# Kernel tuning notes

Measured on AMD Instinct MI355X. Metric: run time of the kernel, lower is better.

Reference implementation:

```python
import jax, jax.numpy as jnp
import numpy as np

B, S, D = 2, 1024, 768      # batch, seq, d_model
F, F_UP = 8192, 8192        # downstream / upstream dictionary sizes
K = 64                      # top-k of the downstream AE
MASK_DENSITY = 0.05         # fraction of allowed feature-feature connections


def setup_inputs() -> dict:
    key = jax.random.key(0)
    ks = jax.random.split(key, 12)
    inv_sqrt_d = 1.0 / np.sqrt(D)
    resid = jax.random.normal(ks[0], (B, S, D), dtype=jnp.float32)
    # upstream pruned features: k-sparse-ish non-negative activations
    pruned0 = jax.nn.relu(jax.random.normal(ks[1], (B, S, F_UP)) - 2.0).astype(jnp.float32)
    pruned1 = jax.nn.relu(jax.random.normal(ks[2], (B, S, F_UP)) - 2.0).astype(jnp.float32)
    feature_buffer = jnp.zeros((B, S, F), dtype=jnp.float32)
    W_enc = jax.random.normal(ks[3], (F, D), dtype=jnp.float32) * inv_sqrt_d
    b_enc = jax.random.normal(ks[4], (F,), dtype=jnp.float32) * 0.01
    W_dec = jax.random.normal(ks[5], (F, D), dtype=jnp.float32) * inv_sqrt_d
    b_dec = jax.random.normal(ks[6], (D,), dtype=jnp.float32) * 0.01
    W_dec_up0 = jax.random.normal(ks[7], (F_UP, D), dtype=jnp.float32) * inv_sqrt_d
    W_dec_up1 = jax.random.normal(ks[8], (F_UP, D), dtype=jnp.float32) * inv_sqrt_d
    b_dec_up0 = jax.random.normal(ks[9], (D,), dtype=jnp.float32) * 0.01
    b_dec_up1 = jax.random.normal(ks[10], (D,), dtype=jnp.float32) * 0.01
    km0, km1 = jax.random.split(ks[11])
    mask0 = (jax.random.uniform(km0, (F, F_UP)) < MASK_DENSITY).astype(jnp.float32)
    mask1 = (jax.random.uniform(km1, (F, F_UP)) < MASK_DENSITY).astype(jnp.float32)
    return {
        "resid": resid, "pruned0": pruned0, "pruned1": pruned1,
        "feature_buffer": feature_buffer,
        "W_enc": W_enc, "b_enc": b_enc, "W_dec": W_dec, "b_dec": b_dec,
        "W_dec_up0": W_dec_up0, "W_dec_up1": W_dec_up1,
        "b_dec_up0": b_dec_up0, "b_dec_up1": b_dec_up1,
        "mask0": mask0, "mask1": mask1, "k": K,
    }


def reference(resid, pruned0, pruned1, feature_buffer,
              W_enc, b_enc, W_dec, b_dec,
              W_dec_up0, W_dec_up1, b_dec_up0, b_dec_up1,
              mask0, mask1, k):
    # initial contributions: encode the cached residual stream, [B,S,F]
    approx = jnp.einsum("bsd,fd->bsf", resid, W_enc)
    upstream_bias = b_dec_up0 + b_dec_up1
    # accumulate connection-masked upstream contributions
    for pruned, W_dec_up, mask in ((pruned0, W_dec_up0, mask0),
                                   (pruned1, W_dec_up1, mask1)):
        # masked virtual weights: [F, F_up]
        virtual = jnp.einsum("fd,ud->fu", W_enc, W_dec_up) * mask
        approx = approx + jnp.einsum("bsu,fu->bsf", pruned, virtual)
    # bias correction: project summed upstream decoder biases, add encoder bias
    approx = approx + jnp.einsum("fd,d->f", W_enc, upstream_bias) + b_enc
    # topk (unsorted set equals torch's sorted=False), relu, scatter into buffer
    top_vals, top_idx = jax.lax.top_k(approx, k)        # [B,S,k]
    top_vals = jax.nn.relu(top_vals)
    Bn, Sn, Fn = feature_buffer.shape
    bi = jnp.arange(Bn)[:, None, None]
    si = jnp.arange(Sn)[None, :, None]
    feat_buffer = jnp.zeros_like(feature_buffer).at[bi, si, top_idx].set(top_vals)
    # dense decode
    reconstructions = jnp.einsum("bsf,fd->bsd", feat_buffer, W_dec) + b_dec
    return feat_buffer, reconstructions
```

## Files before the change

### kernel.cpp

```cpp
#include <hip/hip_runtime.h>
#include <stdint.h>

typedef unsigned long long u64;
typedef unsigned short u16;

#define F_DIM 8192
#define U_DIM 8192
#define D_DIM 768
#define NTOK  2048
#define KSEL  64
#define COLCAP 544
#define TILE  256
#define NFT   32
#define NUT   32
#define DCH   32
#define ENTCAP 3840
#define NBIN  1024

__global__ void k_bias(const float* __restrict__ Wenc, const float* __restrict__ benc,
                       const float* __restrict__ b0, const float* __restrict__ b1,
                       float* __restrict__ t_bias) {
    int wid = threadIdx.x >> 6, lane = threadIdx.x & 63;
    int f = blockIdx.x * 4 + wid;
    const float* row = Wenc + (size_t)f * D_DIM;
    float s = 0.f;
    for (int j = lane; j < D_DIM; j += 64) s += row[j] * (b0[j] + b1[j]);
    #pragma unroll
    for (int off = 32; off; off >>= 1) s += __shfl_down(s, off, 64);
    if (lane == 0) t_bias[f] = s + benc[f];
}

__global__ void k_mask_scan(const float* __restrict__ mask0, const float* __restrict__ mask1,
                            int* __restrict__ cnt_tile, u64* __restrict__ bitmap) {
    int ut = blockIdx.x, ft = blockIdx.y, l = blockIdx.z;
    const float* mask = l ? mask1 : mask0;
    int tid = threadIdx.x, lane = tid & 63, wid = tid >> 6;
    int u = ut * TILE + tid;
    int f0 = ft * TILE;
    u64* bm = bitmap + (((size_t)(l * NFT + ft) * NUT + ut) * TILE) * 4;
    int cnt = 0;
    for (int fl = 0; fl < TILE; ++fl) {
        float v = mask[(size_t)(f0 + fl) * U_DIM + u];
        int nz = (v != 0.0f);
        cnt += nz;
        u64 bal = __ballot(nz);
        if (lane == 0) bm[(size_t)fl * 4 + wid] = bal;
    }
    cnt_tile[(size_t)(l * NFT + ft) * U_DIM + u] = cnt;
}

__global__ void k_col_prefix(const int* __restrict__ cnt_tile, int* __restrict__ base,
                             int* __restrict__ cnt_tot) {
    int idx = blockIdx.x * blockDim.x + threadIdx.x;
    int l = idx >> 13, u = idx & (U_DIM - 1);
    int run = 0;
    for (int ft = 0; ft < NFT; ++ft) {
        int c = cnt_tile[(size_t)(l * NFT + ft) * U_DIM + u];
        base[(size_t)(l * NFT + ft) * U_DIM + u] = run;
        run += c;
    }
    cnt_tot[l * U_DIM + u] = run < COLCAP ? run : COLCAP;
}

__global__ __launch_bounds__(256, 2) void k_virt_build(
        const float* __restrict__ Wenc, const float* __restrict__ Wup0,
        const float* __restrict__ Wup1, const u64* __restrict__ bitmap,
        const int* __restrict__ base, u16* __restrict__ csc_f, float* __restrict__ csc_v) {
    __shared__ u64 bm[TILE][4];
    __shared__ int cs[TILE];
    __shared__ unsigned char entf[ENTCAP];
    __shared__ float acc[ENTCAP];
    __shared__ float we_t[DCH][TILE + 1];
    int ut = blockIdx.x, ft = blockIdx.y, l = blockIdx.z;
    const float* Wup = l ? Wup1 : Wup0;
    int tid = threadIdx.x;
    int u0 = ut * TILE, f0 = ft * TILE;

    const u64* gbm = bitmap + (((size_t)(l * NFT + ft) * NUT + ut) * TILE) * 4;
    for (int i = tid; i < TILE * 4; i += 256) ((u64*)bm)[i] = gbm[i];
    __syncthreads();

    int w = tid >> 6, b = tid & 63;
    int cnt = 0;
    for (int fl = 0; fl < TILE; ++fl) cnt += (int)((bm[fl][w] >> b) & 1ULL);
    cs[tid] = cnt;
    __syncthreads();
    for (int off = 1; off < 256; off <<= 1) {
        int v = (tid >= off) ? cs[tid - off] : 0;
        __syncthreads();
        cs[tid] += v;
        __syncthreads();
    }
    int cstart = cs[tid] - cnt;
    {
        int i = 0;
        for (int fl = 0; fl < TILE; ++fl)
            if ((bm[fl][w] >> b) & 1ULL) {
                int p = cstart + i;
                if (p < ENTCAP) entf[p] = (unsigned char)fl;
                ++i;
            }
    }
    for (int i = tid; i < ENTCAP; i += 256) acc[i] = 0.f;
    __syncthreads();

    float wu[DCH];
    for (int d0 = 0; d0 < D_DIM; d0 += DCH) {
        const float* wr = Wenc + (size_t)(f0 + tid) * D_DIM + d0;
        #pragma unroll
        for (int j = 0; j < DCH; j += 4) {
            float4 t4 = *(const float4*)(wr + j);
            we_t[j][tid] = t4.x; we_t[j + 1][tid] = t4.y;
            we_t[j + 2][tid] = t4.z; we_t[j + 3][tid] = t4.w;
        }
        const float* ur = Wup + (size_t)(u0 + tid) * D_DIM + d0;
        #pragma unroll
        for (int j = 0; j < DCH; j += 4) {
            float4 t4 = *(const float4*)(ur + j);
            wu[j] = t4.x; wu[j + 1] = t4.y; wu[j + 2] = t4.z; wu[j + 3] = t4.w;
        }
        __syncthreads();
        for (int i = 0; i < cnt; ++i) {
            int p = cstart + i;
            if (p >= ENTCAP) break;
            int fl = entf[p];
            float s = 0.f;
            #pragma unroll
            for (int j = 0; j < DCH; ++j) s += we_t[j][fl] * wu[j];
            acc[p] += s;
        }
        __syncthreads();
    }
    int u = u0 + tid;
    int bse = base[(size_t)(l * NFT + ft) * U_DIM + u];
    size_t colbase = ((size_t)l * U_DIM + u) * COLCAP;
    for (int i = 0; i < cnt; ++i) {
        int p = cstart + i;
        if (p >= ENTCAP) break;
        int slot = bse + i;
        if (slot < COLCAP) {
            csc_f[colbase + slot] = (u16)(f0 + entf[p]);
            csc_v[colbase + slot] = acc[p];
        }
    }
}

__global__ __launch_bounds__(512) void k_contrib(
        const float* __restrict__ pruned0, const float* __restrict__ pruned1,
        const int* __restrict__ cnt_tot, const u16* __restrict__ csc_f,
        const float* __restrict__ csc_v, float* __restrict__ C) {
    __shared__ float accum[F_DIM];
    int t = blockIdx.x;
    int tid = threadIdx.x, lane = tid & 63, wid = tid >> 6;
    for (int i = tid; i < F_DIM; i += 512) accum[i] = 0.f;
    __syncthreads();
    for (int l = 0; l < 2; ++l) {
        const float* P = (l ? pruned1 : pruned0) + (size_t)t * U_DIM;
        const int* cl = cnt_tot + l * U_DIM;
        const u16* cf = csc_f + (size_t)l * U_DIM * COLCAP;
        const float* cv = csc_v + (size_t)l * U_DIM * COLCAP;
        for (int w = wid; w < U_DIM / 64; w += 8) {
            float pv = P[w * 64 + lane];
            u64 bal = __ballot(pv != 0.0f);
            while (bal) {
                int bb = __builtin_ctzll(bal);
                bal &= bal - 1;
                int u = w * 64 + bb;
                float p = __shfl(pv, bb, 64);
                int cn = cl[u];
                size_t cb = (size_t)u * COLCAP;
                for (int e = lane; e < cn; e += 64) {
                    int f = cf[cb + e];
                    float v = cv[cb + e];
                    atomicAdd(&accum[f], p * v);
                }
            }
        }
    }
    __syncthreads();
    float* Crow = C + (size_t)t * F_DIM;
    for (int i = tid; i < F_DIM; i += 512) Crow[i] = accum[i];
}

#define BM 128
#define BN 128
#define BK 16
__global__ __launch_bounds__(256) void k_encoder(
        const float* __restrict__ resid, const float* __restrict__ Wenc,
        const float* __restrict__ t_bias, float* __restrict__ C) {
    __shared__ float As[BK][BM + 4];
    __shared__ float Bs[BK][BN + 4];
    int tid = threadIdx.x;
    int m0 = blockIdx.y * BM, n0 = blockIdx.x * BN;
    int mt = tid & 15, nt = tid >> 4;
    float acc[8][8] = {};
    for (int k0 = 0; k0 < D_DIM; k0 += BK) {
        if (tid < 128) {
            const float* ar = resid + (size_t)(m0 + tid) * D_DIM + k0;
            #pragma unroll
            for (int j = 0; j < BK; j += 4) {
                float4 t4 = *(const float4*)(ar + j);
                As[j][tid] = t4.x; As[j + 1][tid] = t4.y;
                As[j + 2][tid] = t4.z; As[j + 3][tid] = t4.w;
            }
        } else {
            int r = tid - 128;
            const float* br = Wenc + (size_t)(n0 + r) * D_DIM + k0;
            #pragma unroll
            for (int j = 0; j < BK; j += 4) {
                float4 t4 = *(const float4*)(br + j);
                Bs[j][r] = t4.x; Bs[j + 1][r] = t4.y;
                Bs[j + 2][r] = t4.z; Bs[j + 3][r] = t4.w;
            }
        }
        __syncthreads();
        #pragma unroll
        for (int k = 0; k < BK; ++k) {
            float a[8], bb[8];
            *(float4*)&a[0]  = *(const float4*)&As[k][mt * 8];
            *(float4*)&a[4]  = *(const float4*)&As[k][mt * 8 + 4];
            *(float4*)&bb[0] = *(const float4*)&Bs[k][nt * 8];
            *(float4*)&bb[4] = *(const float4*)&Bs[k][nt * 8 + 4];
            #pragma unroll
            for (int i = 0; i < 8; ++i)
                #pragma unroll
                for (int j = 0; j < 8; ++j) acc[i][j] += a[i] * bb[j];
        }
        __syncthreads();
    }
    float tb[8];
    #pragma unroll
    for (int j = 0; j < 8; ++j) tb[j] = t_bias[n0 + nt * 8 + j];
    #pragma unroll
    for (int i = 0; i < 8; ++i) {
        float* cr = C + (size_t)(m0 + mt * 8 + i) * F_DIM + n0 + nt * 8;
        #pragma unroll
        for (int j = 0; j < 8; ++j) cr[j] += acc[i][j] + tb[j];
    }
}

__global__ __launch_bounds__(256) void k_select(
        float* __restrict__ C, int* __restrict__ sel_idx, float* __restrict__ sel_val) {
    __shared__ float row[F_DIM];
    __shared__ int hist[NBIN];
    __shared__ int bstar, nsure, ncand;
    __shared__ float sure_v[64];  __shared__ int sure_f[64];
    __shared__ float cand_v[256]; __shared__ int cand_f[256];
    __shared__ float out_v[KSEL]; __shared__ int out_f[KSEL];
    int t = blockIdx.x, tid = threadIdx.x;
    float* Crow = C + (size_t)t * F_DIM;
    for (int i = tid; i < F_DIM; i += 256) row[i] = Crow[i];
    for (int i = tid; i < NBIN; i += 256) hist[i] = 0;
    __syncthreads();
    for (int i = tid; i < F_DIM; i += 256) {
        int b = (int)floorf((row[i] + 16.0f) * 32.0f);
        b = b < 0 ? 0 : (b > NBIN - 1 ? NBIN - 1 : b);
        atomicAdd(&hist[b], 1);
    }
    __syncthreads();
    if (tid == 0) {
        int cum = 0, bs = 0;
        for (int b = NBIN - 1; b >= 0; --b) { cum += hist[b]; if (cum >= KSEL) { bs = b; break; } }
        bstar = bs; nsure = 0; ncand = 0;
    }
    __syncthreads();
    int bs = bstar;
    for (int i = tid; i < F_DIM; i += 256) {
        float v = row[i];
        int b = (int)floorf((v + 16.0f) * 32.0f);
        b = b < 0 ? 0 : (b > NBIN - 1 ? NBIN - 1 : b);
        if (b > bs) {
            int p = atomicAdd(&nsure, 1);
            if (p < 64) { sure_v[p] = v; sure_f[p] = i; }
        } else if (b == bs) {
            int p = atomicAdd(&ncand, 1);
            if (p < 256) { cand_v[p] = v; cand_f[p] = i; }
        }
    }
    __syncthreads();
    if (tid == 0) {
        int c1 = nsure; if (c1 > KSEL) c1 = KSEL;
        for (int i = 0; i < c1; ++i) { out_v[i] = sure_v[i]; out_f[i] = sure_f[i]; }
        int need = KSEL - c1;
        int nc = ncand; if (nc > 256) nc = 256;
        for (int s = 0; s < need; ++s) {
            float bv = -1e30f; int bf = 0x7fffffff, bi = -1;
            for (int i = 0; i < nc; ++i) {
                float v = cand_v[i];
                if (v > bv || (v == bv && cand_f[i] < bf)) { bv = v; bf = cand_f[i]; bi = i; }
            }
            if (bi < 0) { out_v[c1 + s] = 0.f; out_f[c1 + s] = 0; continue; }
            out_v[c1 + s] = cand_v[bi]; out_f[c1 + s] = cand_f[bi];
            cand_v[bi] = -1e30f;
        }
    }
    __syncthreads();
    for (int i = tid; i < F_DIM; i += 256) Crow[i] = 0.0f;
    __syncthreads();
    if (tid < KSEL) {
        float v = out_v[tid]; int f = out_f[tid];
        float rv = v > 0.f ? v : 0.f;
        Crow[f] = rv;
        sel_idx[t * KSEL + tid] = f;
        sel_val[t * KSEL + tid] = rv;
    }
}

__global__ __launch_bounds__(256) void k_decode(
        const int* __restrict__ sel_idx, const float* __restrict__ sel_val,
        const float* __restrict__ Wdec, const float* __restrict__ bdec,
        float* __restrict__ recon) {
    __shared__ int sf[KSEL]; __shared__ float sv[KSEL];
    int t = blockIdx.x, tid = threadIdx.x;
    if (tid < KSEL) { sf[tid] = sel_idx[t * KSEL + tid]; sv[tid] = sel_val[t * KSEL + tid]; }
    __syncthreads();
    for (int d = tid; d < D_DIM; d += 256) {
        float s = bdec[d];
        #pragma unroll 8
        for (int j = 0; j < KSEL; ++j) s += sv[j] * Wdec[(size_t)sf[j] * D_DIM + d];
        recon[(size_t)t * D_DIM + d] = s;
    }
}

extern "C" void kernel_launch(void* const* d_in, const int* in_sizes, int n_in,
                              void* d_out, int out_size, void* d_ws, size_t ws_size,
                              hipStream_t stream) {
    (void)in_sizes; (void)n_in; (void)out_size; (void)ws_size;
    const float* resid   = (const float*)d_in[0];
    const float* pruned0 = (const float*)d_in[1];
    const float* pruned1 = (const float*)d_in[2];
    const float* Wenc    = (const float*)d_in[4];
    const float* benc    = (const float*)d_in[5];
    const float* Wdec    = (const float*)d_in[6];
    const float* bdec    = (const float*)d_in[7];
    const float* Wup0    = (const float*)d_in[8];
    const float* Wup1    = (const float*)d_in[9];
    const float* bup0    = (const float*)d_in[10];
    const float* bup1    = (const float*)d_in[11];
    const float* mask0   = (const float*)d_in[12];
    const float* mask1   = (const float*)d_in[13];

    char* ws = (char*)d_ws;
    size_t o = 0;
    auto alloc = [&](size_t bytes) -> char* {
        o = (o + 255) & ~(size_t)255;
        char* p = ws + o; o += bytes; return p;
    };
    float* t_bias   = (float*)alloc((size_t)F_DIM * 4);
    int*   cnt_tile = (int*)  alloc((size_t)2 * NFT * U_DIM * 4);
    int*   basep    = (int*)  alloc((size_t)2 * NFT * U_DIM * 4);
    int*   cnt_tot  = (int*)  alloc((size_t)2 * U_DIM * 4);
    u64*   bitmap   = (u64*)  alloc((size_t)2 * NFT * NUT * TILE * 4 * 8);
    u16*   csc_f    = (u16*)  alloc((size_t)2 * U_DIM * COLCAP * 2);
    float* csc_v    = (float*)alloc((size_t)2 * U_DIM * COLCAP * 4);
    int*   sel_idx  = (int*)  alloc((size_t)NTOK * KSEL * 4);
    float* sel_val  = (float*)alloc((size_t)NTOK * KSEL * 4);

    float* out   = (float*)d_out;
    float* C     = out;
    float* recon = out + (size_t)NTOK * F_DIM;

    hipLaunchKernelGGL(k_bias,       dim3(F_DIM / 4),        dim3(256), 0, stream,
                       Wenc, benc, bup0, bup1, t_bias);
    hipLaunchKernelGGL(k_mask_scan,  dim3(NUT, NFT, 2),      dim3(256), 0, stream,
                       mask0, mask1, cnt_tile, bitmap);
    hipLaunchKernelGGL(k_col_prefix, dim3(2 * U_DIM / 256),  dim3(256), 0, stream,
                       cnt_tile, basep, cnt_tot);
    hipLaunchKernelGGL(k_virt_build, dim3(NUT, NFT, 2),      dim3(256), 0, stream,
                       Wenc, Wup0, Wup1, bitmap, basep, csc_f, csc_v);
    hipLaunchKernelGGL(k_contrib,    dim3(NTOK),             dim3(512), 0, stream,
                       pruned0, pruned1, cnt_tot, csc_f, csc_v, C);
    hipLaunchKernelGGL(k_encoder,    dim3(F_DIM / BN, NTOK / BM), dim3(256), 0, stream,
                       resid, Wenc, t_bias, C);
    hipLaunchKernelGGL(k_select,     dim3(NTOK),             dim3(256), 0, stream,
                       C, sel_idx, sel_val);
    hipLaunchKernelGGL(k_decode,     dim3(NTOK),             dim3(256), 0, stream,
                       sel_idx, sel_val, Wdec, bdec, recon);
}
```

Measured before the change: 4.322 ms.

## Switch virtual weights to CSR and compute upstream contributions per token-tile/feature-tile

Rebuilds the masked virtual weight matrix as row-major CSR (per downstream feature) instead of CSC, and adds a kernel that collects, for each 128-token tile, a capped list of (token, value) pairs of nonzero upstream activations per upstream feature. The contribution kernel now processes a 128x128 token-by-feature tile in shared memory, walking each feature's CSR row and that tile's token lists, with an XCD-aware block mapping. This is meant to replace a per-token scan of whole CSC columns with scattered atomics over 8192 features by tile-local accumulation with better reuse. The per-tile token list is capped at 16 entries per upstream feature, which may silently drop contributions if activations are denser than expected, and shared-memory atomics remain.

```diff
diff --git a/kernel.cpp b/kernel.cpp
--- a/kernel.cpp
+++ b/kernel.cpp
@@ -9,13 +9,17 @@
 #define D_DIM 768
 #define NTOK  2048
 #define KSEL  64
-#define COLCAP 544
+#define ROWCAP 544
 #define TILE  256
 #define NFT   32
 #define NUT   32
 #define DCH   32
 #define ENTCAP 3840
 #define NBIN  1024
+#define FT    128
+#define TT    128
+#define NTT   16
+#define PCAP  16
 
 __global__ void k_bias(const float* __restrict__ Wenc, const float* __restrict__ benc,
                        const float* __restrict__ b0, const float* __restrict__ b1,
@@ -31,46 +35,46 @@
 }
 
 __global__ void k_mask_scan(const float* __restrict__ mask0, const float* __restrict__ mask1,
-                            int* __restrict__ cnt_tile, u64* __restrict__ bitmap) {
+                            int* __restrict__ rowcnt_tile, u64* __restrict__ bitmap) {
+    __shared__ int rc[TILE][4];
     int ut = blockIdx.x, ft = blockIdx.y, l = blockIdx.z;
     const float* mask = l ? mask1 : mask0;
     int tid = threadIdx.x, lane = tid & 63, wid = tid >> 6;
     int u = ut * TILE + tid;
     int f0 = ft * TILE;
     u64* bm = bitmap + (((size_t)(l * NFT + ft) * NUT + ut) * TILE) * 4;
-    int cnt = 0;
     for (int fl = 0; fl < TILE; ++fl) {
         float v = mask[(size_t)(f0 + fl) * U_DIM + u];
-        int nz = (v != 0.0f);
-        cnt += nz;
-        u64 bal = __ballot(nz);
-        if (lane == 0) bm[(size_t)fl * 4 + wid] = bal;
-    }
-    cnt_tile[(size_t)(l * NFT + ft) * U_DIM + u] = cnt;
-}
-
-__global__ void k_col_prefix(const int* __restrict__ cnt_tile, int* __restrict__ base,
-                             int* __restrict__ cnt_tot) {
+        u64 bal = __ballot(v != 0.0f);
+        if (lane == 0) { bm[(size_t)fl * 4 + wid] = bal; rc[fl][wid] = __popcll(bal); }
+    }
+    __syncthreads();
+    rowcnt_tile[(size_t)(l * NUT + ut) * F_DIM + f0 + tid] =
+        rc[tid][0] + rc[tid][1] + rc[tid][2] + rc[tid][3];
+}
+
+__global__ void k_row_prefix(const int* __restrict__ rowcnt_tile, int* __restrict__ base_r,
+                             int* __restrict__ rowcnt_tot) {
     int idx = blockIdx.x * blockDim.x + threadIdx.x;
-    int l = idx >> 13, u = idx & (U_DIM - 1);
+    int l = idx >> 13, f = idx & (F_DIM - 1);
     int run = 0;
-    for (int ft = 0; ft < NFT; ++ft) {
-        int c = cnt_tile[(size_t)(l * NFT + ft) * U_DIM + u];
-        base[(size_t)(l * NFT + ft) * U_DIM + u] = run;
+    for (int ut = 0; ut < NUT; ++ut) {
+        int c = rowcnt_tile[(size_t)(l * NUT + ut) * F_DIM + f];
+        base_r[(size_t)(l * NUT + ut) * F_DIM + f] = run;
         run += c;
     }
-    cnt_tot[l * U_DIM + u] = run < COLCAP ? run : COLCAP;
+    rowcnt_tot[l * F_DIM + f] = run < ROWCAP ? run : ROWCAP;
 }
 
 __global__ __launch_bounds__(256, 2) void k_virt_build(
         const float* __restrict__ Wenc, const float* __restrict__ Wup0,
         const float* __restrict__ Wup1, const u64* __restrict__ bitmap,
-        const int* __restrict__ base, u16* __restrict__ csc_f, float* __restrict__ csc_v) {
+        const int* __restrict__ base_r, u16* __restrict__ csr_u, float* __restrict__ csr_v) {
     __shared__ u64 bm[TILE][4];
     __shared__ int cs[TILE];
-    __shared__ unsigned char entf[ENTCAP];
+    __shared__ unsigned char entu[ENTCAP];
     __shared__ float acc[ENTCAP];
-    __shared__ float we_t[DCH][TILE + 1];
+    __shared__ float wu_t[DCH][TILE + 1];
     int ut = blockIdx.x, ft = blockIdx.y, l = blockIdx.z;
     const float* Wup = l ? Wup1 : Wup0;
     int tid = threadIdx.x;
@@ -80,9 +84,9 @@
     for (int i = tid; i < TILE * 4; i += 256) ((u64*)bm)[i] = gbm[i];
     __syncthreads();
 
-    int w = tid >> 6, b = tid & 63;
     int cnt = 0;
-    for (int fl = 0; fl < TILE; ++fl) cnt += (int)((bm[fl][w] >> b) & 1ULL);
+    #pragma unroll
+    for (int w = 0; w < 4; ++w) cnt += (int)__popcll(bm[tid][w]);
     cs[tid] = cnt;
     __syncthreads();
     for (int off = 1; off < 256; off <<= 1) {
@@ -94,92 +98,131 @@
     int cstart = cs[tid] - cnt;
     {
         int i = 0;
-        for (int fl = 0; fl < TILE; ++fl)
-            if ((bm[fl][w] >> b) & 1ULL) {
+        #pragma unroll
+        for (int w = 0; w < 4; ++w) {
+            u64 word = bm[tid][w];
+            while (word) {
+                int b = __builtin_ctzll(word); word &= word - 1;
                 int p = cstart + i;
-                if (p < ENTCAP) entf[p] = (unsigned char)fl;
+                if (p < ENTCAP) entu[p] = (unsigned char)(w * 64 + b);
                 ++i;
             }
+        }
     }
     for (int i = tid; i < ENTCAP; i += 256) acc[i] = 0.f;
     __syncthreads();
 
-    float wu[DCH];
+    float we[DCH];
     for (int d0 = 0; d0 < D_DIM; d0 += DCH) {
+        const float* ur = Wup + (size_t)(u0 + tid) * D_DIM + d0;
+        #pragma unroll
+        for (int j = 0; j < DCH; j += 4) {
+            float4 t4 = *(const float4*)(ur + j);
+            wu_t[j][tid] = t4.x; wu_t[j + 1][tid] = t4.y;
+            wu_t[j + 2][tid] = t4.z; wu_t[j + 3][tid] = t4.w;
+        }
         const float* wr = Wenc + (size_t)(f0 + tid) * D_DIM + d0;
         #pragma unroll
         for (int j = 0; j < DCH; j += 4) {
             float4 t4 = *(const float4*)(wr + j);
-            we_t[j][tid] = t4.x; we_t[j + 1][tid] = t4.y;
-            we_t[j + 2][tid] = t4.z; we_t[j + 3][tid] = t4.w;
-        }
-        const float* ur = Wup + (size_t)(u0 + tid) * D_DIM + d0;
-        #pragma unroll
-        for (int j = 0; j < DCH; j += 4) {
-            float4 t4 = *(const float4*)(ur + j);
-            wu[j] = t4.x; wu[j + 1] = t4.y; wu[j + 2] = t4.z; wu[j + 3] = t4.w;
+            we[j] = t4.x; we[j + 1] = t4.y; we[j + 2] = t4.z; we[j + 3] = t4.w;
         }
         __syncthreads();
         for (int i = 0; i < cnt; ++i) {
             int p = cstart + i;
             if (p >= ENTCAP) break;
-            int fl = entf[p];
+            int ul = entu[p];
             float s = 0.f;
             #pragma unroll
-            for (int j = 0; j < DCH; ++j) s += we_t[j][fl] * wu[j];
+            for (int j = 0; j < DCH; ++j) s += we[j] * wu_t[j][ul];
             acc[p] += s;
         }
         __syncthreads();
     }
-    int u = u0 + tid;
-    int bse = base[(size_t)(l * NFT + ft) * U_DIM + u];
-    size_t colbase = ((size_t)l * U_DIM + u) * COLCAP;
+    int f = f0 + tid;
+    int bse = base_r[(size_t)(l * NUT + ut) * F_DIM + f];
+    size_t rb = ((size_t)l * F_DIM + f) * ROWCAP;
     for (int i = 0; i < cnt; ++i) {
         int p = cstart + i;
         if (p >= ENTCAP) break;
         int slot = bse + i;
-        if (slot < COLCAP) {
-            csc_f[colbase + slot] = (u16)(f0 + entf[p]);
-            csc_v[colbase + slot] = acc[p];
-        }
-    }
-}
-
-__global__ __launch_bounds__(512) void k_contrib(
+        if (slot < ROWCAP) {
+            csr_u[rb + slot] = (u16)(u0 + entu[p]);
+            csr_v[rb + slot] = acc[p];
+        }
+    }
+}
+
+__global__ __launch_bounds__(256) void k_ptok(
         const float* __restrict__ pruned0, const float* __restrict__ pruned1,
-        const int* __restrict__ cnt_tot, const u16* __restrict__ csc_f,
-        const float* __restrict__ csc_v, float* __restrict__ C) {
-    __shared__ float accum[F_DIM];
-    int t = blockIdx.x;
+        u64* __restrict__ lists, unsigned char* __restrict__ cnt8) {
+    __shared__ int cl[U_DIM];
+    int tt = blockIdx.x, l = blockIdx.y;
+    int tid = threadIdx.x;
+    for (int i = tid; i < U_DIM; i += 256) cl[i] = 0;
+    __syncthreads();
+    const float* P = (l ? pruned1 : pruned0) + (size_t)tt * TT * U_DIM;
+    u64* L = lists + (size_t)(l * NTT + tt) * U_DIM * PCAP;
+    for (int t = 0; t < TT; ++t) {
+        const float* Pr = P + (size_t)t * U_DIM;
+        for (int u = tid; u < U_DIM; u += 256) {
+            float v = Pr[u];
+            if (v != 0.0f) {
+                int c = atomicAdd(&cl[u], 1);
+                if (c < PCAP)
+                    L[(size_t)u * PCAP + c] = ((u64)__float_as_uint(v) << 32) | (unsigned)t;
+            }
+        }
+    }
+    __syncthreads();
+    unsigned char* C8 = cnt8 + (size_t)(l * NTT + tt) * U_DIM;
+    for (int u = tid; u < U_DIM; u += 256) {
+        int c = cl[u];
+        C8[u] = (unsigned char)(c < PCAP ? c : PCAP);
+    }
+}
+
+__global__ __launch_bounds__(512, 2) void k_contrib2(
+        const u16* __restrict__ csr_u, const float* __restrict__ csr_v,
+        const int* __restrict__ rowcnt_tot, const u64* __restrict__ lists,
+        const unsigned char* __restrict__ cnt8, float* __restrict__ C) {
+    __shared__ float accum[TT][FT + 1];
+    __shared__ unsigned char lc[U_DIM];
+    int raw = blockIdx.x;
+    int xcd = raw & 7, idx = raw >> 3;
+    int ft = (xcd << 3) | (idx & 7);
+    int tt = idx >> 3;
     int tid = threadIdx.x, lane = tid & 63, wid = tid >> 6;
-    for (int i = tid; i < F_DIM; i += 512) accum[i] = 0.f;
-    __syncthreads();
+    for (int i = tid; i < TT * (FT + 1); i += 512) ((float*)accum)[i] = 0.f;
     for (int l = 0; l < 2; ++l) {
-        const float* P = (l ? pruned1 : pruned0) + (size_t)t * U_DIM;
-        const int* cl = cnt_tot + l * U_DIM;
-        const u16* cf = csc_f + (size_t)l * U_DIM * COLCAP;
-        const float* cv = csc_v + (size_t)l * U_DIM * COLCAP;
-        for (int w = wid; w < U_DIM / 64; w += 8) {
-            float pv = P[w * 64 + lane];
-            u64 bal = __ballot(pv != 0.0f);
-            while (bal) {
-                int bb = __builtin_ctzll(bal);
-                bal &= bal - 1;
-                int u = w * 64 + bb;
-                float p = __shfl(pv, bb, 64);
-                int cn = cl[u];
-                size_t cb = (size_t)u * COLCAP;
-                for (int e = lane; e < cn; e += 64) {
-                    int f = cf[cb + e];
-                    float v = cv[cb + e];
-                    atomicAdd(&accum[f], p * v);
+        __syncthreads();
+        for (int i = tid; i < U_DIM; i += 512) lc[i] = cnt8[(size_t)(l * NTT + tt) * U_DIM + i];
+        __syncthreads();
+        const u64* L = lists + (size_t)(l * NTT + tt) * U_DIM * PCAP;
+        for (int r = wid; r < FT; r += 8) {
+            int f = ft * FT + r;
+            int cnt = rowcnt_tot[l * F_DIM + f];
+            size_t rb = ((size_t)l * F_DIM + f) * ROWCAP;
+            for (int e = lane; e < cnt; e += 64) {
+                int u = csr_u[rb + e];
+                float v = csr_v[rb + e];
+                int c = lc[u];
+                const u64* lp = L + (size_t)u * PCAP;
+                for (int j = 0; j < c; ++j) {
+                    u64 pk = lp[j];
+                    int tok = (int)(unsigned)pk;
+                    float p = __uint_as_float((unsigned)(pk >> 32));
+                    atomicAdd(&accum[tok][r], p * v);
                 }
             }
         }
     }
     __syncthreads();
-    float* Crow = C + (size_t)t * F_DIM;
-    for (int i = tid; i < F_DIM; i += 512) Crow[i] = accum[i];
+    int t0 = tt * TT, f0 = ft * FT;
+    for (int i = tid; i < TT * FT; i += 512) {
+        int tok = i >> 7, r = i & (FT - 1);
+        C[(size_t)(t0 + tok) * F_DIM + f0 + r] = accum[tok][r];
+    }
 }
 
 #define BM 128
@@ -346,15 +389,17 @@
         o = (o + 255) & ~(size_t)255;
         char* p = ws + o; o += bytes; return p;
     };
-    float* t_bias   = (float*)alloc((size_t)F_DIM * 4);
-    int*   cnt_tile = (int*)  alloc((size_t)2 * NFT * U_DIM * 4);
-    int*   basep    = (int*)  alloc((size_t)2 * NFT * U_DIM * 4);
-    int*   cnt_tot  = (int*)  alloc((size_t)2 * U_DIM * 4);
-    u64*   bitmap   = (u64*)  alloc((size_t)2 * NFT * NUT * TILE * 4 * 8);
-    u16*   csc_f    = (u16*)  alloc((size_t)2 * U_DIM * COLCAP * 2);
-    float* csc_v    = (float*)alloc((size_t)2 * U_DIM * COLCAP * 4);
-    int*   sel_idx  = (int*)  alloc((size_t)NTOK * KSEL * 4);
-    float* sel_val  = (float*)alloc((size_t)NTOK * KSEL * 4);
+    float* t_bias      = (float*)alloc((size_t)F_DIM * 4);
+    int*   rowcnt_tile = (int*)  alloc((size_t)2 * NUT * F_DIM * 4);
+    int*   base_r      = (int*)  alloc((size_t)2 * NUT * F_DIM * 4);
+    int*   rowcnt_tot  = (int*)  alloc((size_t)2 * F_DIM * 4);
+    u64*   bitmap      = (u64*)  alloc((size_t)2 * NFT * NUT * TILE * 4 * 8);
+    u16*   csr_u       = (u16*)  alloc((size_t)2 * F_DIM * ROWCAP * 2);
+    float* csr_v       = (float*)alloc((size_t)2 * F_DIM * ROWCAP * 4);
+    u64*   lists       = (u64*)  alloc((size_t)2 * NTT * U_DIM * PCAP * 8);
+    unsigned char* cnt8 = (unsigned char*)alloc((size_t)2 * NTT * U_DIM);
+    int*   sel_idx     = (int*)  alloc((size_t)NTOK * KSEL * 4);
+    float* sel_val     = (float*)alloc((size_t)NTOK * KSEL * 4);
 
     float* out   = (float*)d_out;
     float* C     = out;
@@ -363,13 +408,15 @@
     hipLaunchKernelGGL(k_bias,       dim3(F_DIM / 4),        dim3(256), 0, stream,
                        Wenc, benc, bup0, bup1, t_bias);
     hipLaunchKernelGGL(k_mask_scan,  dim3(NUT, NFT, 2),      dim3(256), 0, stream,
-                       mask0, mask1, cnt_tile, bitmap);
-    hipLaunchKernelGGL(k_col_prefix, dim3(2 * U_DIM / 256),  dim3(256), 0, stream,
-                       cnt_tile, basep, cnt_tot);
+                       mask0, mask1, rowcnt_tile, bitmap);
+    hipLaunchKernelGGL(k_row_prefix, dim3(2 * F_DIM / 256),  dim3(256), 0, stream,
+                       rowcnt_tile, base_r, rowcnt_tot);
     hipLaunchKernelGGL(k_virt_build, dim3(NUT, NFT, 2),      dim3(256), 0, stream,
-                       Wenc, Wup0, Wup1, bitmap, basep, csc_f, csc_v);
-    hipLaunchKernelGGL(k_contrib,    dim3(NTOK),             dim3(512), 0, stream,
-                       pruned0, pruned1, cnt_tot, csc_f, csc_v, C);
+                       Wenc, Wup0, Wup1, bitmap, base_r, csr_u, csr_v);
+    hipLaunchKernelGGL(k_ptok,       dim3(NTT, 2),           dim3(256), 0, stream,
+                       pruned0, pruned1, lists, cnt8);
+    hipLaunchKernelGGL(k_contrib2,   dim3(8 * 8 * NTT),      dim3(512), 0, stream,
+                       csr_u, csr_v, rowcnt_tot, lists, cnt8, C);
     hipLaunchKernelGGL(k_encoder,    dim3(F_DIM / BN, NTOK / BM), dim3(256), 0, stream,
                        resid, Wenc, t_bias, C);
     hipLaunchKernelGGL(k_select,     dim3(NTOK),             dim3(256), 0, stream,
```

After: 6.301 ms. 45.8% more time.
